# Optimization experiments

Hardware: AMD Instinct MI355X
Metric: run time of the kernel (lower is better)

## Reference

```python
import jax, jax.numpy as jnp
import numpy as np

F_DIM, HID, H, DQ, DV = 1024, 4096, 16, 64, 64
EPS = 1e-6

def layer_norm(x, w, b):
    mu = jnp.mean(x, axis=-1, keepdims=True)
    var = jnp.mean(jnp.square(x - mu), axis=-1, keepdims=True)
    return (x - mu) * jax.lax.rsqrt(var + EPS) * w + b

def setup_inputs() -> dict:
    key = jax.random.key(0)
    ks = jax.random.split(key, 8)
    s = 0.02
    return {
        'x': jax.random.normal(ks[0], (4, 2048, F_DIM), dtype=jnp.float32),
        'ln1_w': jnp.ones((F_DIM,), jnp.float32),
        'ln1_b': jnp.zeros((F_DIM,), jnp.float32),
        'wq_w': jax.random.normal(ks[1], (H * DQ, F_DIM), jnp.float32) * s,
        'wq_b': jnp.zeros((H * DQ,), jnp.float32),
        'wk_w': jax.random.normal(ks[2], (H * DQ, F_DIM), jnp.float32) * s,
        'wk_b': jnp.zeros((H * DQ,), jnp.float32),
        'wv_w': jax.random.normal(ks[3], (H * DV, F_DIM), jnp.float32) * s,
        'wv_b': jnp.zeros((H * DV,), jnp.float32),
        'fc_w': jax.random.normal(ks[4], (F_DIM, H * DV), jnp.float32) * s,
        'fc_b': jnp.zeros((F_DIM,), jnp.float32),
        'ln2_w': jnp.ones((F_DIM,), jnp.float32),
        'ln2_b': jnp.zeros((F_DIM,), jnp.float32),
        'fc1_w': jax.random.normal(ks[5], (HID, F_DIM), jnp.float32) * s,
        'fc1_b': jnp.zeros((HID,), jnp.float32),
        'fc2_w': jax.random.normal(ks[6], (F_DIM, HID), jnp.float32) * s,
        'fc2_b': jnp.zeros((F_DIM,), jnp.float32),
    }

def reference(x, ln1_w, ln1_b, wq_w, wq_b, wk_w, wk_b, wv_w, wv_b,
              fc_w, fc_b, ln2_w, ln2_b, fc1_w, fc1_b, fc2_w, fc2_b):
    B, S, _ = x.shape
    # --- pre-LN multi-head self-attention ---
    h = layer_norm(x, ln1_w, ln1_b)
    q = (h @ wq_w.T + wq_b).reshape(B, S, H, DQ).transpose(0, 2, 1, 3)  # [B,H,S,dq]
    k = (h @ wk_w.T + wk_b).reshape(B, S, H, DQ).transpose(0, 2, 1, 3)
    v = (h @ wv_w.T + wv_b).reshape(B, S, H, DV).transpose(0, 2, 1, 3)
    attn = jax.nn.softmax(jnp.einsum('bhqd,bhkd->bhqk', q, k) / jnp.sqrt(jnp.float32(DQ)), axis=-1)
    out = jnp.einsum('bhqk,bhkd->bhqd', attn, v).transpose(0, 2, 1, 3).reshape(B, S, H * DV)
    x = x + (out @ fc_w.T + fc_b)
    # --- pre-LN residual MLP ---
    h2 = layer_norm(x, ln2_w, ln2_b)
    ff = jax.nn.relu(h2 @ fc1_w.T + fc1_b) @ fc2_w.T + fc2_b
    return x + ff
```

## Files before the change

### kernel.cpp

```cpp
#include <hip/hip_runtime.h>

#define F_DIMC 1024
#define HIDC   4096
#define NH     16
#define SEQ    2048
#define BATCH  4
#define ROWS   (BATCH * SEQ)
#define MEG    (1u << 20)
#define QSCALE 0.18033688011112042f

typedef unsigned short u16t;
typedef __attribute__((ext_vector_type(8))) short short8;
typedef __attribute__((ext_vector_type(4))) float floatx4;
typedef __attribute__((address_space(1))) void gvoid_t;
typedef __attribute__((address_space(3))) void lvoid_t;
#define ASYNC16(g, l) __builtin_amdgcn_global_load_lds((gvoid_t*)(g), (lvoid_t*)(l), 16, 0, 0)

#if __has_builtin(__builtin_amdgcn_exp2f)
#define EXP2(x) __builtin_amdgcn_exp2f(x)
#else
#define EXP2(x) exp2f(x)
#endif

__device__ __forceinline__ u16t f2bf(float f) {
    union { float f; unsigned u; } v; v.f = f;
    unsigned r = v.u + 0x7fffu + ((v.u >> 16) & 1u);
    return (u16t)(r >> 16);
}
__device__ __forceinline__ unsigned fasu(float f) {
    union { float f; unsigned u; } v; v.f = f; return v.u;
}

__global__ __launch_bounds__(256) void ln_kernel(const float* __restrict__ x,
                                                 const float* __restrict__ w,
                                                 const float* __restrict__ b,
                                                 u16t* __restrict__ out) {
    const int row = blockIdx.x;
    const int t = threadIdx.x;
    const float* xp = x + (size_t)row * F_DIMC;

    float4 v = *(const float4*)(xp + t * 4);
    float s  = v.x + v.y + v.z + v.w;
    float ss = v.x * v.x + v.y * v.y + v.z * v.z + v.w * v.w;
    for (int off = 32; off; off >>= 1) {
        s  += __shfl_down(s, off);
        ss += __shfl_down(ss, off);
    }
    __shared__ float red[8];
    const int wid = t >> 6, lid = t & 63;
    if (lid == 0) { red[wid] = s; red[4 + wid] = ss; }
    __syncthreads();
    if (t == 0) {
        float S  = red[0] + red[1] + red[2] + red[3];
        float SS = red[4] + red[5] + red[6] + red[7];
        float mu  = S * (1.0f / F_DIMC);
        float var = SS * (1.0f / F_DIMC) - mu * mu;
        red[0] = mu;
        red[1] = rsqrtf(var + 1e-6f);
    }
    __syncthreads();
    const float mu = red[0], rs = red[1];

    float4 wv = *(const float4*)(w + t * 4);
    float4 bv = *(const float4*)(b + t * 4);
    ushort4 o = make_ushort4(f2bf((v.x - mu) * rs * wv.x + bv.x),
                             f2bf((v.y - mu) * rs * wv.y + bv.y),
                             f2bf((v.z - mu) * rs * wv.z + bv.z),
                             f2bf((v.w - mu) * rs * wv.w + bv.w));
    *(ushort4*)(out + (size_t)row * F_DIMC + t * 4) = o;
}

__global__ __launch_bounds__(256) void wconv_kernel(const float* __restrict__ w0,
        const float* __restrict__ w1, const float* __restrict__ w2,
        const float* __restrict__ w3, const float* __restrict__ w4,
        const float* __restrict__ w5, u16t* __restrict__ dst) {
    const size_t e = ((size_t)blockIdx.x * 256 + threadIdx.x) * 4;
    const float* src; size_t off;
    if      (e < 1 * MEG) { src = w0; off = e; }
    else if (e < 2 * MEG) { src = w1; off = e - 1 * MEG; }
    else if (e < 3 * MEG) { src = w2; off = e - 2 * MEG; }
    else if (e < 4 * MEG) { src = w3; off = e - 3 * MEG; }
    else if (e < 8 * MEG) { src = w4; off = e - 4 * MEG; }
    else                  { src = w5; off = e - 8 * MEG; }
    float4 f = *(const float4*)(src + off);
    *(ushort4*)(dst + e) = make_ushort4(f2bf(f.x), f2bf(f.y), f2bf(f.z), f2bf(f.w));
}

#define DP_PROLOGUE_AND_LOOP(Aq, Wq, Kdim, NBX)                                \
    __shared__ u16t As[2][256 * 64] __attribute__((aligned(16)));              \
    __shared__ u16t Ws[2][128 * 64] __attribute__((aligned(16)));              \
    const int t = threadIdx.x;                                                 \
    const int lane = t & 63;                                                   \
    const int wave = t >> 6;                                                   \
    const int wm = wave >> 1, wn = wave & 1;                                   \
    const int fm = lane & 15, fq = lane >> 4;                                  \
    const int l7 = lane & 7;                                                   \
         \
    const int nwg = gridDim.x;                                                 \
    const int swzb = (blockIdx.x & 7) * (nwg >> 3) + (blockIdx.x >> 3);        \
    const int m0 = (swzb / (NBX)) * 256, n0 = (swzb % (NBX)) * 128;            \
               \
    const u16t* ag[4]; const u16t* wg2[2];                                     \
    int alo[4]; int wlo[2];                                                    \
    _Pragma("unroll")                                                          \
    for (int i = 0; i < 4; ++i) {                                              \
        const int beta = i * 512 + t;                                          \
        const int r = beta >> 3, j = (beta & 7) ^ (r & 7);                     \
        ag[i] = (Aq) + (size_t)(m0 + r) * (Kdim) + j * 8;                      \
        alo[i] = beta * 8;                                                     \
    }                                                                          \
    _Pragma("unroll")                                                          \
    for (int i = 0; i < 2; ++i) {                                              \
        const int beta = i * 512 + t;                                          \
        const int r = beta >> 3, j = (beta & 7) ^ (r & 7);                     \
        wg2[i] = (Wq) + (size_t)(n0 + r) * (Kdim) + j * 8;                     \
        wlo[i] = beta * 8;                                                     \
    }                                                                          \
          \
    int abase[2], bbase[2];                                                    \
    _Pragma("unroll")                                                          \
    for (int ks = 0; ks < 2; ++ks) {                                           \
        const int sw = (ks * 4 + fq) ^ l7;                                     \
        abase[ks] = (wm * 64 + fm) * 64 + sw * 8;                              \
        bbase[ks] = (wn * 64 + fm) * 64 + sw * 8;                              \
    }                                                                          \
    const int NT = (Kdim) / 64;                                                \
                       \
    _Pragma("unroll")                                                          \
    for (int i = 0; i < 4; ++i) ASYNC16(ag[i], &As[0][alo[i]]);                \
    _Pragma("unroll")                                                          \
    for (int i = 0; i < 2; ++i) ASYNC16(wg2[i], &Ws[0][wlo[i]]);               \
    _Pragma("unroll")                                                          \
    for (int i = 0; i < 4; ++i) ASYNC16(ag[i] + 64, &As[1][alo[i]]);           \
    _Pragma("unroll")                                                          \
    for (int i = 0; i < 2; ++i) ASYNC16(wg2[i] + 64, &Ws[1][wlo[i]]);          \
    _Pragma("unroll")                                                          \
    for (int i = 0; i < 4; ++i) ag[i] += 128;                                  \
    _Pragma("unroll")                                                          \
    for (int i = 0; i < 2; ++i) wg2[i] += 128;                                 \
    asm volatile("s_waitcnt vmcnt(6)" ::: "memory");         \
    __builtin_amdgcn_s_barrier();                                              \
    __builtin_amdgcn_sched_barrier(0);                                         \
    floatx4 acc[4][4] = {};                                                    \
    for (int tt = 0; tt < NT; ++tt) {                                          \
        const u16t* Ab = As[tt & 1];                                           \
        const u16t* Wb = Ws[tt & 1];                                           \
                                      \
        short8 fa[4], fb[4];                                                   \
        _Pragma("unroll")                                                      \
        for (int mi = 0; mi < 4; ++mi)                                         \
            fa[mi] = *(const short8*)(Ab + abase[0] + mi * 1024);              \
        _Pragma("unroll")                                                      \
        for (int ni = 0; ni < 4; ++ni)                                         \
            fb[ni] = *(const short8*)(Wb + bbase[0] + ni * 1024);              \
        __builtin_amdgcn_s_setprio(1);                                         \
        _Pragma("unroll")                                                      \
        for (int mi = 0; mi < 4; ++mi)                                         \
            _Pragma("unroll")                                                  \
            for (int ni = 0; ni < 4; ++ni)                                     \
                acc[mi][ni] = __builtin_amdgcn_mfma_f32_16x16x32_bf16(         \
                    fa[mi], fb[ni], acc[mi][ni], 0, 0, 0);                     \
        __builtin_amdgcn_s_setprio(0);                                         \
                     \
        short8 fa1[4], fb1[4];                                                 \
        _Pragma("unroll")                                                      \
        for (int mi = 0; mi < 4; ++mi)                                         \
            fa1[mi] = *(const short8*)(Ab + abase[1] + mi * 1024);             \
        _Pragma("unroll")                                                      \
        for (int ni = 0; ni < 4; ++ni)                                         \
            fb1[ni] = *(const short8*)(Wb + bbase[1] + ni * 1024);             \
        asm volatile("s_waitcnt lgkmcnt(0)" ::: "memory");  \
        __builtin_amdgcn_s_barrier();        \
        __builtin_amdgcn_sched_barrier(0);                                     \
        if (tt + 2 < NT) {                                                     \
            const int pb = tt & 1;           \
            _Pragma("unroll")                                                  \
            for (int i = 0; i < 4; ++i) {                                      \
                ASYNC16(ag[i], &As[pb][alo[i]]); ag[i] += 64;                  \
            }                                                                  \
            _Pragma("unroll")                                                  \
            for (int i = 0; i < 2; ++i) {                                      \
                ASYNC16(wg2[i], &Ws[pb][wlo[i]]); wg2[i] += 64;                \
            }                                                                  \
                  \
            asm volatile("s_waitcnt vmcnt(6)" ::: "memory");                   \
        } else {                                                               \
            asm volatile("s_waitcnt vmcnt(0)" ::: "memory");                   \
        }                                                                      \
        __builtin_amdgcn_s_barrier();                                          \
        __builtin_amdgcn_sched_barrier(0);                                     \
              \
        __builtin_amdgcn_s_setprio(1);                                         \
        _Pragma("unroll")                                                      \
        for (int mi = 0; mi < 4; ++mi)                                         \
            _Pragma("unroll")                                                  \
            for (int ni = 0; ni < 4; ++ni)                                     \
                acc[mi][ni] = __builtin_amdgcn_mfma_f32_16x16x32_bf16(         \
                    fa1[mi], fb1[ni], acc[mi][ni], 0, 0, 0);                   \
        __builtin_amdgcn_s_setprio(0);                                         \
    }

template <bool RELU, bool RES, bool BF16OUT>
__global__ __launch_bounds__(512, 2) void gemm_dp(const u16t* __restrict__ A,
                                                  const u16t* __restrict__ W,
                                                  const float* __restrict__ bias,
                                                  const float* res, void* Cout,
                                                  int N, int K) {
    DP_PROLOGUE_AND_LOOP(A, W, K, N / 128)
    float bl[4];
#pragma unroll
    for (int ni = 0; ni < 4; ++ni) bl[ni] = bias[n0 + wn * 64 + ni * 16 + fm];
#pragma unroll
    for (int mi = 0; mi < 4; ++mi) {
#pragma unroll
        for (int ni = 0; ni < 4; ++ni) {
            const int col = n0 + wn * 64 + ni * 16 + fm;
#pragma unroll
            for (int r = 0; r < 4; ++r) {
                const int row = m0 + wm * 64 + mi * 16 + fq * 4 + r;
                const size_t off = (size_t)row * N + col;
                float c = acc[mi][ni][r] + bl[ni];
                if (RELU) c = fmaxf(c, 0.0f);
                if (RES)  c += res[off];
                if (BF16OUT) ((u16t*)Cout)[off] = f2bf(c);
                else         ((float*)Cout)[off] = c;
            }
        }
    }
}

__global__ __launch_bounds__(512, 2) void gemm_qkv(const u16t* __restrict__ A,
        const u16t* __restrict__ W,
        const float* __restrict__ wq_b, const float* __restrict__ wk_b,
        const float* __restrict__ wv_b,
        u16t* __restrict__ qb, u16t* __restrict__ kb, u16t* __restrict__ vtb) {
    DP_PROLOGUE_AND_LOOP(A, W, F_DIMC, 3072 / 128)
    const int which = n0 >> 10;
    const int nb = n0 & 1023;
    const float* bias = which == 0 ? wq_b : which == 1 ? wk_b : wv_b;
    float bl[4];
#pragma unroll
    for (int ni = 0; ni < 4; ++ni) bl[ni] = bias[nb + wn * 64 + ni * 16 + fm];

    if (which == 2) {
#pragma unroll
        for (int mi = 0; mi < 4; ++mi)
#pragma unroll
            for (int ni = 0; ni < 4; ++ni) {
                const int col = nb + wn * 64 + ni * 16 + fm;
                const int row0 = m0 + wm * 64 + mi * 16 + fq * 4;
                ushort4 pk = make_ushort4(f2bf(acc[mi][ni][0] + bl[ni]),
                                          f2bf(acc[mi][ni][1] + bl[ni]),
                                          f2bf(acc[mi][ni][2] + bl[ni]),
                                          f2bf(acc[mi][ni][3] + bl[ni]));
                *(ushort4*)(vtb + (size_t)col * ROWS + row0) = pk;
            }
    } else {
        u16t* dst = (which == 0) ? qb : kb;
        const float sc2 = (which == 0) ? QSCALE : 1.0f;
#pragma unroll
        for (int mi = 0; mi < 4; ++mi)
#pragma unroll
            for (int ni = 0; ni < 4; ++ni) {
                const int col = nb + wn * 64 + ni * 16 + fm;
#pragma unroll
                for (int r = 0; r < 4; ++r) {
                    const int row = m0 + wm * 64 + mi * 16 + fq * 4 + r;
                    dst[(size_t)row * F_DIMC + col] = f2bf((acc[mi][ni][r] + bl[ni]) * sc2);
                }
            }
    }
}

__global__ __launch_bounds__(256, 4) void attn_mfma(const u16t* __restrict__ qb,
        const u16t* __restrict__ kbuf, const u16t* __restrict__ vtb,
        u16t* __restrict__ ab) {
    __shared__ u16t Kt[2][64 * 64] __attribute__((aligned(16)));
    __shared__ u16t Vs[64 * 64] __attribute__((aligned(16)));
    __shared__ u16t QP[128 * 64] __attribute__((aligned(16)));

    const int t = threadIdx.x;
    const int lane = t & 63;
    const int wave = t >> 6;
    const int l15 = lane & 15, q4 = lane >> 4;
    const int q0 = blockIdx.x * 128;
    const int bh = blockIdx.y;
    const int b = bh >> 4, hh = bh & 15;

#pragma unroll
    for (int c = 0; c < 4; ++c) {
        const int beta = c * 256 + t;
        const int r = beta >> 3, o = (beta & 7) ^ (r & 7);
        ASYNC16(qb + (size_t)(b * SEQ + q0 + r) * F_DIMC + hh * 64 + o * 8,
                QP + beta * 8);
    }
    const u16t* kg = kbuf + (size_t)(b * SEQ) * F_DIMC + hh * 64;
    const u16t* vg = vtb + (size_t)(hh * 64) * ROWS + b * SEQ;

    const int sb0 = t, sb1 = t + 256;
    const int sr0 = sb0 >> 3, so0 = (sb0 & 7) ^ (sr0 & 7);
    const int sr1 = sb1 >> 3, so1 = (sb1 & 7) ^ (sr1 & 7);
    const u16t* kp0 = kg + (size_t)sr0 * F_DIMC + so0 * 8;
    const u16t* kp1 = kg + (size_t)sr1 * F_DIMC + so1 * 8;
    const u16t* vp0 = vg + (size_t)sr0 * ROWS + so0 * 8;
    const u16t* vp1 = vg + (size_t)sr1 * ROWS + so1 * 8;

    ASYNC16(kp0, Kt[0] + sb0 * 8);
    ASYNC16(kp1, Kt[0] + sb1 * 8);
    ASYNC16(vp0, Vs + sb0 * 8);
    ASYNC16(vp1, Vs + sb1 * 8);
    kp0 += 64 * F_DIMC; kp1 += 64 * F_DIMC; vp0 += 64; vp1 += 64;
    __syncthreads();

    short8 fqr[2][2];
#pragma unroll
    for (int mt = 0; mt < 2; ++mt)
#pragma unroll
        for (int ks = 0; ks < 2; ++ks) {
            const int m = wave * 32 + mt * 16 + l15;
            const int oct = ks * 4 + q4;
            fqr[mt][ks] = *(const short8*)(QP + (m * 8 + (oct ^ (m & 7))) * 8);
        }

    short8 ones;
#pragma unroll
    for (int i = 0; i < 8; ++i) ones[i] = (short)0x3F80;

    floatx4 oacc[2][4] = {};
    floatx4 lacc[2] = {};

    for (int it = 0; it < SEQ / 64; ++it) {
        if (it + 1 < SEQ / 64) {
            u16t* kd = Kt[(it + 1) & 1];
            ASYNC16(kp0, kd + sb0 * 8);
            ASYNC16(kp1, kd + sb1 * 8);
            kp0 += 64 * F_DIMC; kp1 += 64 * F_DIMC;
        }
        const u16t* kcur = Kt[it & 1];

        short8 fk[4][2];
#pragma unroll
        for (int nt = 0; nt < 4; ++nt)
#pragma unroll
            for (int ks = 0; ks < 2; ++ks) {
                const int kr = nt * 16 + l15;
                const int oct = ks * 4 + q4;
                fk[nt][ks] = *(const short8*)(kcur + (kr * 8 + (oct ^ (kr & 7))) * 8);
            }
        floatx4 st[2][4] = {};
#pragma unroll
        for (int mt = 0; mt < 2; ++mt)
#pragma unroll
            for (int nt = 0; nt < 4; ++nt) {
                st[mt][nt] = __builtin_amdgcn_mfma_f32_16x16x32_bf16(
                    fk[nt][0], fqr[mt][0], st[mt][nt], 0, 0, 0);
                st[mt][nt] = __builtin_amdgcn_mfma_f32_16x16x32_bf16(
                    fk[nt][1], fqr[mt][1], st[mt][nt], 0, 0, 0);
            }

#pragma unroll
        for (int mt = 0; mt < 2; ++mt)
#pragma unroll
            for (int nt = 0; nt < 4; ++nt) {
                const float p0 = EXP2(st[mt][nt][0]);
                const float p1 = EXP2(st[mt][nt][1]);
                const float p2 = EXP2(st[mt][nt][2]);
                const float p3 = EXP2(st[mt][nt][3]);
                const unsigned lo = __builtin_amdgcn_perm(fasu(p1), fasu(p0), 0x07060302u);
                const unsigned hi = __builtin_amdgcn_perm(fasu(p3), fasu(p2), 0x07060302u);
                const int m = wave * 32 + mt * 16 + l15;
                const int logb = nt * 2 + (q4 >> 1);
                *(uint2*)(QP + (m * 8 + (logb ^ (m & 7))) * 8 + (q4 & 1) * 4) =
                    make_uint2(lo, hi);
            }

        asm volatile("s_waitcnt lgkmcnt(0)" ::: "memory");
        if (it + 1 < SEQ / 64) {
            asm volatile("s_waitcnt vmcnt(2)" ::: "memory");
        } else {
            asm volatile("s_waitcnt vmcnt(0)" ::: "memory");
        }
        __builtin_amdgcn_s_barrier();

        short8 fp[2][2], fv[4][2];
#pragma unroll
        for (int mt = 0; mt < 2; ++mt)
#pragma unroll
            for (int ks = 0; ks < 2; ++ks) {
                const int m = wave * 32 + mt * 16 + l15;
                const int oct = ks * 4 + q4;
                fp[mt][ks] = *(const short8*)(QP + (m * 8 + (oct ^ (m & 7))) * 8);
            }
#pragma unroll
        for (int nd = 0; nd < 4; ++nd)
#pragma unroll
            for (int ks = 0; ks < 2; ++ks) {
                const int d = nd * 16 + l15;
                const int oct = ks * 4 + q4;
                fv[nd][ks] = *(const short8*)(Vs + (d * 8 + (oct ^ (d & 7))) * 8);
            }
#pragma unroll
        for (int mt = 0; mt < 2; ++mt) {
#pragma unroll
            for (int nd = 0; nd < 4; ++nd) {
                oacc[mt][nd] = __builtin_amdgcn_mfma_f32_16x16x32_bf16(
                    fp[mt][0], fv[nd][0], oacc[mt][nd], 0, 0, 0);
                oacc[mt][nd] = __builtin_amdgcn_mfma_f32_16x16x32_bf16(
                    fp[mt][1], fv[nd][1], oacc[mt][nd], 0, 0, 0);
            }
            lacc[mt] = __builtin_amdgcn_mfma_f32_16x16x32_bf16(
                fp[mt][0], ones, lacc[mt], 0, 0, 0);
            lacc[mt] = __builtin_amdgcn_mfma_f32_16x16x32_bf16(
                fp[mt][1], ones, lacc[mt], 0, 0, 0);
        }

        asm volatile("s_waitcnt lgkmcnt(0)" ::: "memory");
        asm volatile("s_waitcnt vmcnt(0)" ::: "memory");
        __builtin_amdgcn_s_barrier();
        if (it + 1 < SEQ / 64) {
            ASYNC16(vp0, Vs + sb0 * 8);
            ASYNC16(vp1, Vs + sb1 * 8);
            vp0 += 64; vp1 += 64;
        }
    }

#pragma unroll
    for (int mt = 0; mt < 2; ++mt) {
        floatx4 rinv;
#pragma unroll
        for (int r = 0; r < 4; ++r) rinv[r] = 1.0f / lacc[mt][r];
#pragma unroll
        for (int nd = 0; nd < 4; ++nd)
#pragma unroll
            for (int r = 0; r < 4; ++r) {
                const int row = b * SEQ + q0 + wave * 32 + mt * 16 + q4 * 4 + r;
                const int col = hh * 64 + nd * 16 + l15;
                ab[(size_t)row * F_DIMC + col] = f2bf(oacc[mt][nd][r] * rinv[r]);
            }
    }
}

extern "C" void kernel_launch(void* const* d_in, const int* in_sizes, int n_in,
                              void* d_out, int out_size, void* d_ws, size_t ws_size,
                              hipStream_t stream) {
    const float* x     = (const float*)d_in[0];
    const float* ln1_w = (const float*)d_in[1];
    const float* ln1_b = (const float*)d_in[2];
    const float* wq_w  = (const float*)d_in[3];
    const float* wq_b  = (const float*)d_in[4];
    const float* wk_w  = (const float*)d_in[5];
    const float* wk_b  = (const float*)d_in[6];
    const float* wv_w  = (const float*)d_in[7];
    const float* wv_b  = (const float*)d_in[8];
    const float* fc_w  = (const float*)d_in[9];
    const float* fc_b  = (const float*)d_in[10];
    const float* ln2_w = (const float*)d_in[11];
    const float* ln2_b = (const float*)d_in[12];
    const float* fc1_w = (const float*)d_in[13];
    const float* fc1_b = (const float*)d_in[14];
    const float* fc2_w = (const float*)d_in[15];
    const float* fc2_b = (const float*)d_in[16];

    float* out = (float*)d_out;
    u16t*  ws  = (u16t*)d_ws;

    u16t* wbuf = ws;
    u16t* bwqkv = wbuf;
    u16t* bwfc = wbuf + 3 * MEG;
    u16t* bwf1 = wbuf + 4 * MEG;
    u16t* bwf2 = wbuf + 8 * MEG;
    u16t* h    = wbuf + 12 * MEG;
    u16t* qb   = h + 8 * MEG;
    u16t* kb   = qb + 8 * MEG;
    u16t* vtb  = kb + 8 * MEG;
    u16t* ab   = vtb + 8 * MEG;
    u16t* ff   = qb;

    const dim3 blk(256);
    const dim3 blk512(512);
    const int gQKV = (ROWS / 256) * (3072 / 128);
    const int gF   = (ROWS / 256) * (F_DIMC / 128);
    const int gH   = (ROWS / 256) * (HIDC / 128);

    wconv_kernel<<<12 * MEG / 1024, blk, 0, stream>>>(wq_w, wk_w, wv_w, fc_w, fc1_w, fc2_w, wbuf);
    ln_kernel<<<ROWS, blk, 0, stream>>>(x, ln1_w, ln1_b, h);
    gemm_qkv<<<gQKV, blk512, 0, stream>>>(h, bwqkv, wq_b, wk_b, wv_b, qb, kb, vtb);
    attn_mfma<<<dim3(SEQ / 128, BATCH * NH), blk, 0, stream>>>(qb, kb, vtb, ab);
    gemm_dp<false, true, false><<<gF, blk512, 0, stream>>>(ab, bwfc, fc_b, x, out, F_DIMC, F_DIMC);
    ln_kernel<<<ROWS, blk, 0, stream>>>(out, ln2_w, ln2_b, h);
    gemm_dp<true, false, true><<<gH, blk512, 0, stream>>>(h, bwf1, fc1_b, nullptr, ff, HIDC, F_DIMC);
    gemm_dp<false, true, false><<<gF, blk512, 0, stream>>>(ff, bwf2, fc2_b, out, out, F_DIMC, HIDC);
}
```

Before: 514.0 us.

## Use 256x256 block tiles for QKV and FC1 GEMMs

Adds a wider GEMM variant in which each 512-thread block computes a 256x256 output tile, with each wave owning 128x64 and 32 accumulators, instead of 256x128. The QKV projection and FC1 GEMMs switch to it, which halves their grid sizes. The aim is more MFMA work per LDS fragment load and less redundant global traffic for A. In exchange it doubles LDS use to 128KB per block and raises register pressure, which can reduce occupancy below the declared two blocks per CU and leaves fewer blocks to fill the CUs.

```diff
diff --git a/kernel.cpp b/kernel.cpp
--- a/kernel.cpp
+++ b/kernel.cpp
@@ -95,11 +95,9 @@
     const int wm = wave >> 1, wn = wave & 1;                                   \
     const int fm = lane & 15, fq = lane >> 4;                                  \
     const int l7 = lane & 7;                                                   \
-         \
     const int nwg = gridDim.x;                                                 \
     const int swzb = (blockIdx.x & 7) * (nwg >> 3) + (blockIdx.x >> 3);        \
     const int m0 = (swzb / (NBX)) * 256, n0 = (swzb % (NBX)) * 128;            \
-               \
     const u16t* ag[4]; const u16t* wg2[2];                                     \
     int alo[4]; int wlo[2];                                                    \
     _Pragma("unroll")                                                          \
@@ -116,7 +114,6 @@
         wg2[i] = (Wq) + (size_t)(n0 + r) * (Kdim) + j * 8;                     \
         wlo[i] = beta * 8;                                                     \
     }                                                                          \
-          \
     int abase[2], bbase[2];                                                    \
     _Pragma("unroll")                                                          \
     for (int ks = 0; ks < 2; ++ks) {                                           \
@@ -125,7 +122,6 @@
         bbase[ks] = (wn * 64 + fm) * 64 + sw * 8;                              \
     }                                                                          \
     const int NT = (Kdim) / 64;                                                \
-                       \
     _Pragma("unroll")                                                          \
     for (int i = 0; i < 4; ++i) ASYNC16(ag[i], &As[0][alo[i]]);                \
     _Pragma("unroll")                                                          \
@@ -138,14 +134,13 @@
     for (int i = 0; i < 4; ++i) ag[i] += 128;                                  \
     _Pragma("unroll")                                                          \
     for (int i = 0; i < 2; ++i) wg2[i] += 128;                                 \
-    asm volatile("s_waitcnt vmcnt(6)" ::: "memory");         \
+    asm volatile("s_waitcnt vmcnt(6)" ::: "memory");                           \
     __builtin_amdgcn_s_barrier();                                              \
     __builtin_amdgcn_sched_barrier(0);                                         \
     floatx4 acc[4][4] = {};                                                    \
     for (int tt = 0; tt < NT; ++tt) {                                          \
         const u16t* Ab = As[tt & 1];                                           \
         const u16t* Wb = Ws[tt & 1];                                           \
-                                      \
         short8 fa[4], fb[4];                                                   \
         _Pragma("unroll")                                                      \
         for (int mi = 0; mi < 4; ++mi)                                         \
@@ -156,34 +151,130 @@
         __builtin_amdgcn_s_setprio(1);                                         \
         _Pragma("unroll")                                                      \
         for (int mi = 0; mi < 4; ++mi)                                         \
+            _Pragma("unroll")                                                  \
+            for (int ni = 0; ni < 4; ++ni)                                     \
+                acc[mi][ni] = __builtin_amdgcn_mfma_f32_16x16x32_bf16(         \
+                    fa[mi], fb[ni], acc[mi][ni], 0, 0, 0);                     \
+        __builtin_amdgcn_s_setprio(0);                                         \
+        short8 fa1[4], fb1[4];                                                 \
+        _Pragma("unroll")                                                      \
+        for (int mi = 0; mi < 4; ++mi)                                         \
+            fa1[mi] = *(const short8*)(Ab + abase[1] + mi * 1024);             \
+        _Pragma("unroll")                                                      \
+        for (int ni = 0; ni < 4; ++ni)                                         \
+            fb1[ni] = *(const short8*)(Wb + bbase[1] + ni * 1024);             \
+        asm volatile("s_waitcnt lgkmcnt(0)" ::: "memory");                     \
+        __builtin_amdgcn_s_barrier();                                          \
+        __builtin_amdgcn_sched_barrier(0);                                     \
+        if (tt + 2 < NT) {                                                     \
+            const int pb = tt & 1;                                             \
+            _Pragma("unroll")                                                  \
+            for (int i = 0; i < 4; ++i) {                                      \
+                ASYNC16(ag[i], &As[pb][alo[i]]); ag[i] += 64;                  \
+            }                                                                  \
+            _Pragma("unroll")                                                  \
+            for (int i = 0; i < 2; ++i) {                                      \
+                ASYNC16(wg2[i], &Ws[pb][wlo[i]]); wg2[i] += 64;                \
+            }                                                                  \
+            asm volatile("s_waitcnt vmcnt(6)" ::: "memory");                   \
+        } else {                                                               \
+            asm volatile("s_waitcnt vmcnt(0)" ::: "memory");                   \
+        }                                                                      \
+        __builtin_amdgcn_s_barrier();                                          \
+        __builtin_amdgcn_sched_barrier(0);                                     \
+        __builtin_amdgcn_s_setprio(1);                                         \
+        _Pragma("unroll")                                                      \
+        for (int mi = 0; mi < 4; ++mi)                                         \
+            _Pragma("unroll")                                                  \
+            for (int ni = 0; ni < 4; ++ni)                                     \
+                acc[mi][ni] = __builtin_amdgcn_mfma_f32_16x16x32_bf16(         \
+                    fa1[mi], fb1[ni], acc[mi][ni], 0, 0, 0);                   \
+        __builtin_amdgcn_s_setprio(0);                                         \
+    }
+
+#define DPW_PROLOGUE_AND_LOOP(Aq, Wq, Kdim, NBX)                               \
+    __shared__ u16t As[2][256 * 64] __attribute__((aligned(16)));              \
+    __shared__ u16t Bs[2][256 * 64] __attribute__((aligned(16)));              \
+    const int t = threadIdx.x;                                                 \
+    const int lane = t & 63;                                                   \
+    const int wave = t >> 6;                                                   \
+    const int wr = wave >> 2, wc = wave & 3;                                   \
+    const int fm = lane & 15, fq = lane >> 4;                                  \
+    const int l7 = lane & 7;                                                   \
+    const int nwg = gridDim.x;                                                 \
+    const int swzb = (blockIdx.x & 7) * (nwg >> 3) + (blockIdx.x >> 3);        \
+    const int m0 = (swzb / (NBX)) * 256, n0 = (swzb % (NBX)) * 256;            \
+    const u16t* ag[4]; const u16t* bg[4];                                      \
+    int alo[4]; int blo[4];                                                    \
+    _Pragma("unroll")                                                          \
+    for (int i = 0; i < 4; ++i) {                                              \
+        const int beta = i * 512 + t;                                          \
+        const int r = beta >> 3, j = (beta & 7) ^ (r & 7);                     \
+        ag[i] = (Aq) + (size_t)(m0 + r) * (Kdim) + j * 8;                      \
+        bg[i] = (Wq) + (size_t)(n0 + r) * (Kdim) + j * 8;                      \
+        alo[i] = beta * 8; blo[i] = beta * 8;                                  \
+    }                                                                          \
+    int abase[2], bbase[2];                                                    \
+    _Pragma("unroll")                                                          \
+    for (int ks = 0; ks < 2; ++ks) {                                           \
+        const int sw = (ks * 4 + fq) ^ l7;                                     \
+        abase[ks] = (wr * 128 + fm) * 64 + sw * 8;                             \
+        bbase[ks] = (wc * 64 + fm) * 64 + sw * 8;                              \
+    }                                                                          \
+    const int NT = (Kdim) / 64;                                                \
+    _Pragma("unroll")                                                          \
+    for (int i = 0; i < 4; ++i) ASYNC16(ag[i], &As[0][alo[i]]);                \
+    _Pragma("unroll")                                                          \
+    for (int i = 0; i < 4; ++i) ASYNC16(bg[i], &Bs[0][blo[i]]);                \
+    _Pragma("unroll")                                                          \
+    for (int i = 0; i < 4; ++i) { ASYNC16(ag[i] + 64, &As[1][alo[i]]); ag[i] += 128; } \
+    _Pragma("unroll")                                                          \
+    for (int i = 0; i < 4; ++i) { ASYNC16(bg[i] + 64, &Bs[1][blo[i]]); bg[i] += 128; } \
+    asm volatile("s_waitcnt vmcnt(8)" ::: "memory");         \
+    __builtin_amdgcn_s_barrier();                                              \
+    __builtin_amdgcn_sched_barrier(0);                                         \
+    floatx4 acc[8][4] = {};                                                    \
+    for (int tt = 0; tt < NT; ++tt) {                                          \
+        const u16t* Ab = As[tt & 1];                                           \
+        const u16t* Bb = Bs[tt & 1];                                           \
+                                      \
+        short8 fa[8], fb[4];                                                   \
+        _Pragma("unroll")                                                      \
+        for (int mi = 0; mi < 8; ++mi)                                         \
+            fa[mi] = *(const short8*)(Ab + abase[0] + mi * 1024);              \
+        _Pragma("unroll")                                                      \
+        for (int ni = 0; ni < 4; ++ni)                                         \
+            fb[ni] = *(const short8*)(Bb + bbase[0] + ni * 1024);              \
+        __builtin_amdgcn_s_setprio(1);                                         \
+        _Pragma("unroll")                                                      \
+        for (int mi = 0; mi < 8; ++mi)                                         \
             _Pragma("unroll")                                                  \
             for (int ni = 0; ni < 4; ++ni)                                     \
                 acc[mi][ni] = __builtin_amdgcn_mfma_f32_16x16x32_bf16(         \
                     fa[mi], fb[ni], acc[mi][ni], 0, 0, 0);                     \
         __builtin_amdgcn_s_setprio(0);                                         \
                      \
-        short8 fa1[4], fb1[4];                                                 \
-        _Pragma("unroll")                                                      \
-        for (int mi = 0; mi < 4; ++mi)                                         \
+        short8 fa1[8], fb1[4];                                                 \
+        _Pragma("unroll")                                                      \
+        for (int mi = 0; mi < 8; ++mi)                                         \
             fa1[mi] = *(const short8*)(Ab + abase[1] + mi * 1024);             \
         _Pragma("unroll")                                                      \
         for (int ni = 0; ni < 4; ++ni)                                         \
-            fb1[ni] = *(const short8*)(Wb + bbase[1] + ni * 1024);             \
-        asm volatile("s_waitcnt lgkmcnt(0)" ::: "memory");  \
-        __builtin_amdgcn_s_barrier();        \
+            fb1[ni] = *(const short8*)(Bb + bbase[1] + ni * 1024);             \
+        asm volatile("s_waitcnt lgkmcnt(0)" ::: "memory");                     \
+        __builtin_amdgcn_s_barrier();                                          \
         __builtin_amdgcn_sched_barrier(0);                                     \
         if (tt + 2 < NT) {                                                     \
-            const int pb = tt & 1;           \
+            const int pb = tt & 1;                                             \
             _Pragma("unroll")                                                  \
             for (int i = 0; i < 4; ++i) {                                      \
                 ASYNC16(ag[i], &As[pb][alo[i]]); ag[i] += 64;                  \
             }                                                                  \
             _Pragma("unroll")                                                  \
-            for (int i = 0; i < 2; ++i) {                                      \
-                ASYNC16(wg2[i], &Ws[pb][wlo[i]]); wg2[i] += 64;                \
+            for (int i = 0; i < 4; ++i) {                                      \
+                ASYNC16(bg[i], &Bs[pb][blo[i]]); bg[i] += 64;                  \
             }                                                                  \
-                  \
-            asm volatile("s_waitcnt vmcnt(6)" ::: "memory");                   \
+            asm volatile("s_waitcnt vmcnt(8)" ::: "memory");                   \
         } else {                                                               \
             asm volatile("s_waitcnt vmcnt(0)" ::: "memory");                   \
         }                                                                      \
@@ -192,7 +283,7 @@
               \
         __builtin_amdgcn_s_setprio(1);                                         \
         _Pragma("unroll")                                                      \
-        for (int mi = 0; mi < 4; ++mi)                                         \
+        for (int mi = 0; mi < 8; ++mi)                                         \
             _Pragma("unroll")                                                  \
             for (int ni = 0; ni < 4; ++ni)                                     \
                 acc[mi][ni] = __builtin_amdgcn_mfma_f32_16x16x32_bf16(         \
@@ -229,26 +320,55 @@
     }
 }
 
+template <bool RELU, bool RES, bool BF16OUT>
+__global__ __launch_bounds__(512, 2) void gemm_dpw(const u16t* __restrict__ A,
+                                                   const u16t* __restrict__ W,
+                                                   const float* __restrict__ bias,
+                                                   const float* res, void* Cout,
+                                                   int N, int K) {
+    DPW_PROLOGUE_AND_LOOP(A, W, K, N / 256)
+    float bl[4];
+#pragma unroll
+    for (int ni = 0; ni < 4; ++ni) bl[ni] = bias[n0 + wc * 64 + ni * 16 + fm];
+#pragma unroll
+    for (int mi = 0; mi < 8; ++mi) {
+#pragma unroll
+        for (int ni = 0; ni < 4; ++ni) {
+            const int col = n0 + wc * 64 + ni * 16 + fm;
+#pragma unroll
+            for (int r = 0; r < 4; ++r) {
+                const int row = m0 + wr * 128 + mi * 16 + fq * 4 + r;
+                const size_t off = (size_t)row * N + col;
+                float c = acc[mi][ni][r] + bl[ni];
+                if (RELU) c = fmaxf(c, 0.0f);
+                if (RES)  c += res[off];
+                if (BF16OUT) ((u16t*)Cout)[off] = f2bf(c);
+                else         ((float*)Cout)[off] = c;
+            }
+        }
+    }
+}
+
 __global__ __launch_bounds__(512, 2) void gemm_qkv(const u16t* __restrict__ A,
         const u16t* __restrict__ W,
         const float* __restrict__ wq_b, const float* __restrict__ wk_b,
         const float* __restrict__ wv_b,
         u16t* __restrict__ qb, u16t* __restrict__ kb, u16t* __restrict__ vtb) {
-    DP_PROLOGUE_AND_LOOP(A, W, F_DIMC, 3072 / 128)
+    DPW_PROLOGUE_AND_LOOP(A, W, F_DIMC, 3072 / 256)
     const int which = n0 >> 10;
     const int nb = n0 & 1023;
     const float* bias = which == 0 ? wq_b : which == 1 ? wk_b : wv_b;
     float bl[4];
 #pragma unroll
-    for (int ni = 0; ni < 4; ++ni) bl[ni] = bias[nb + wn * 64 + ni * 16 + fm];
+    for (int ni = 0; ni < 4; ++ni) bl[ni] = bias[nb + wc * 64 + ni * 16 + fm];
 
     if (which == 2) {
 #pragma unroll
-        for (int mi = 0; mi < 4; ++mi)
+        for (int mi = 0; mi < 8; ++mi)
 #pragma unroll
             for (int ni = 0; ni < 4; ++ni) {
-                const int col = nb + wn * 64 + ni * 16 + fm;
-                const int row0 = m0 + wm * 64 + mi * 16 + fq * 4;
+                const int col = nb + wc * 64 + ni * 16 + fm;
+                const int row0 = m0 + wr * 128 + mi * 16 + fq * 4;
                 ushort4 pk = make_ushort4(f2bf(acc[mi][ni][0] + bl[ni]),
                                           f2bf(acc[mi][ni][1] + bl[ni]),
                                           f2bf(acc[mi][ni][2] + bl[ni]),
@@ -259,13 +379,13 @@
         u16t* dst = (which == 0) ? qb : kb;
         const float sc2 = (which == 0) ? QSCALE : 1.0f;
 #pragma unroll
-        for (int mi = 0; mi < 4; ++mi)
+        for (int mi = 0; mi < 8; ++mi)
 #pragma unroll
             for (int ni = 0; ni < 4; ++ni) {
-                const int col = nb + wn * 64 + ni * 16 + fm;
+                const int col = nb + wc * 64 + ni * 16 + fm;
 #pragma unroll
                 for (int r = 0; r < 4; ++r) {
-                    const int row = m0 + wm * 64 + mi * 16 + fq * 4 + r;
+                    const int row = m0 + wr * 128 + mi * 16 + fq * 4 + r;
                     dst[(size_t)row * F_DIMC + col] = f2bf((acc[mi][ni][r] + bl[ni]) * sc2);
                 }
             }
@@ -478,9 +598,9 @@
 
     const dim3 blk(256);
     const dim3 blk512(512);
-    const int gQKV = (ROWS / 256) * (3072 / 128);
+    const int gQKV = (ROWS / 256) * (3072 / 256);
     const int gF   = (ROWS / 256) * (F_DIMC / 128);
-    const int gH   = (ROWS / 256) * (HIDC / 128);
+    const int gH   = (ROWS / 256) * (HIDC / 256);
 
     wconv_kernel<<<12 * MEG / 1024, blk, 0, stream>>>(wq_w, wk_w, wv_w, fc_w, fc1_w, fc2_w, wbuf);
     ln_kernel<<<ROWS, blk, 0, stream>>>(x, ln1_w, ln1_b, h);
@@ -488,6 +608,6 @@
     attn_mfma<<<dim3(SEQ / 128, BATCH * NH), blk, 0, stream>>>(qb, kb, vtb, ab);
     gemm_dp<false, true, false><<<gF, blk512, 0, stream>>>(ab, bwfc, fc_b, x, out, F_DIMC, F_DIMC);
     ln_kernel<<<ROWS, blk, 0, stream>>>(out, ln2_w, ln2_b, h);
-    gemm_dp<true, false, true><<<gH, blk512, 0, stream>>>(h, bwf1, fc1_b, nullptr, ff, HIDC, F_DIMC);
+    gemm_dpw<true, false, true><<<gH, blk512, 0, stream>>>(h, bwf1, fc1_b, nullptr, ff, HIDC, F_DIMC);
     gemm_dp<false, true, false><<<gF, blk512, 0, stream>>>(ff, bwf2, fc2_b, out, out, F_DIMC, HIDC);
 }
```

Measured after the change: 500.0 us. 1.03x faster.
